# Kernel optimization log

Hardware: AMD Instinct MI355X
Metric: run time of the kernel (lower is better)

Reference implementation:

```python
import jax, jax.numpy as jnp
import numpy as np

H = 16        # num_attention_heads
DH = 64       # attention_head_dim
D = H * DH    # model dim = 1024
FF = 4 * D    # feed-forward inner dim = 4096
SCALE = DH ** -0.5
EPS = 1e-12


def _ln(x, g, b):
    m = jnp.mean(x, axis=-1, keepdims=True)
    v = jnp.mean((x - m) ** 2, axis=-1, keepdims=True)
    return (x - m) * jax.lax.rsqrt(v + EPS) * g + b


def _attn(x, ctx, Wq, Wk, Wv, Wo, bo, mask):
    # x: [B,S,D] (already pre-normed), ctx: [B,T,D], mask: [B,T] int (1=keep) or None
    B, S, _ = x.shape
    T = ctx.shape[1]
    q = (x @ Wq).reshape(B, S, H, DH)
    k = (ctx @ Wk).reshape(B, T, H, DH)
    v = (ctx @ Wv).reshape(B, T, H, DH)
    scores = jnp.einsum('bqhd,bkhd->bhqk', q, k) * SCALE  # [B,H,S,T]
    if mask is not None:
        scores = jnp.where(mask[:, None, None, :] == 0, -jnp.inf, scores)
    probs = jax.nn.softmax(scores, axis=-1)
    out = jnp.einsum('bhqk,bkhd->bqhd', probs, v).reshape(B, S, D)
    return out @ Wo + bo


def _geglu_ff(x, Wff1, bff1, Wff2, bff2):
    y = x @ Wff1 + bff1                 # [B,S,2*FF]
    h, gate = y[..., :FF], y[..., FF:]
    # GEGLU computes exact (erf) gelu in fp32
    g = jax.nn.gelu(gate.astype(jnp.float32), approximate=False).astype(gate.dtype)
    return (h * g) @ Wff2 + bff2


def setup_inputs() -> dict:
    key = jax.random.key(0)
    ks = jax.random.split(key, 24)
    B, S, T = 4, 1024, 1024
    w = lambda k, shp: jax.random.normal(k, shp, dtype=jnp.float32) * 0.02
    inp = {
        'hidden_states': jax.random.normal(ks[0], (B, S, D), dtype=jnp.float32),
        'context': jax.random.normal(ks[1], (B, T, D), dtype=jnp.float32),
        'encoder_key_padding_mask': jnp.ones((B, T), dtype=jnp.int32),
        'g1': jnp.ones((D,), jnp.float32), 'b1': jnp.zeros((D,), jnp.float32),
        'g2': jnp.ones((D,), jnp.float32), 'b2': jnp.zeros((D,), jnp.float32),
        'g3': jnp.ones((D,), jnp.float32), 'b3': jnp.zeros((D,), jnp.float32),
        'Wq1': w(ks[2], (D, D)), 'Wk1': w(ks[3], (D, D)), 'Wv1': w(ks[4], (D, D)),
        'Wo1': w(ks[5], (D, D)), 'bo1': jnp.zeros((D,), jnp.float32),
        'Wq2': w(ks[6], (D, D)), 'Wk2': w(ks[7], (D, D)), 'Wv2': w(ks[8], (D, D)),
        'Wo2': w(ks[9], (D, D)), 'bo2': jnp.zeros((D,), jnp.float32),
        'Wff1': w(ks[10], (D, 2 * FF)), 'bff1': jnp.zeros((2 * FF,), jnp.float32),
        'Wff2': w(ks[11], (FF, D)), 'bff2': jnp.zeros((D,), jnp.float32),
    }
    return inp


def reference(hidden_states, context, encoder_key_padding_mask,
              g1, b1, g2, b2, g3, b3,
              Wq1, Wk1, Wv1, Wo1, bo1,
              Wq2, Wk2, Wv2, Wo2, bo2,
              Wff1, bff1, Wff2, bff2):
    # Self-attention (attn1): context defaults to (normed) hidden_states, no padding mask
    n1 = _ln(hidden_states, g1, b1)
    h = hidden_states + _attn(n1, n1, Wq1, Wk1, Wv1, Wo1, bo1, None)
    # Cross-attention (attn2) with encoder key padding mask
    n2 = _ln(h, g2, b2)
    h = h + _attn(n2, context, Wq2, Wk2, Wv2, Wo2, bo2, encoder_key_padding_mask)
    # GEGLU feed-forward
    h = h + _geglu_ff(_ln(h, g3, b3), Wff1, bff1, Wff2, bff2)
    return h
```

## Files before the change

### kernel.cpp

```cpp
#include <hip/hip_runtime.h>

typedef unsigned short u16;
typedef unsigned int u32;

#define B_ 4
#define S_ 1024
#define D_ 1024
#define H_ 16
#define DH_ 64
#define FF_ 4096
#define M_ 4096
#define SCALE_ 0.125f

typedef __attribute__((ext_vector_type(8))) __bf16 bf16x8;
typedef __attribute__((ext_vector_type(4))) float f32x4;

__device__ __forceinline__ f32x4 mfma16(bf16x8 a, bf16x8 b, f32x4 c) {
  return __builtin_amdgcn_mfma_f32_16x16x32_bf16(a, b, c, 0, 0, 0);
}

__device__ __forceinline__ u16 f2bf(float x) {
  union { __bf16 h; u16 u; } cv; cv.h = (__bf16)x; return cv.u;
}
__device__ __forceinline__ float bf2f(u16 u) {
  union { u32 u; float f; } cv; cv.u = ((u32)u) << 16; return cv.f;
}
__device__ __forceinline__ u32 packbf2(float a, float b) {
  union { u32 u; __bf16 h[2]; } pk;
  pk.h[0] = (__bf16)a; pk.h[1] = (__bf16)b;
  return pk.u;
}
__device__ __forceinline__ float gelu_exact(float x) {
  return 0.5f * x * (1.f + erff(x * 0.7071067811865475f));
}
__device__ __forceinline__ void gload16(const void* g, void* l) {
  __builtin_amdgcn_global_load_lds((__attribute__((address_space(1))) void*)(g),
                                   (__attribute__((address_space(3))) void*)(l),
                                   16, 0, 0);
}

template<int EPI>
__global__ __launch_bounds__(256, 2) void gemm128(
    const u16* __restrict__ A, const u16* __restrict__ BT,
    const float* __restrict__ bias, const float* __restrict__ res,
    void* __restrict__ out, int M, int N, int K, int ktiles)
{
  __shared__ u16 As[2][128 * 64];
  __shared__ u16 Bs[2][128 * 64];

  const int tid = threadIdx.x;
  const int wave = tid >> 6, lane = tid & 63;
  const int wm = wave >> 1, wn = wave & 1;
  const int qi = lane & 15, g = lane >> 4;

  const int gx = N >> 7;
  const int nwg = gx * (M >> 7);
  int id = blockIdx.y * gridDim.x + blockIdx.x;
  id = (id & 7) * (nwg >> 3) + (id >> 3);
  const int m0 = (id / gx) << 7, n0 = (id % gx) << 7;

  const int NT = ktiles;
  const int kbase = blockIdx.z * ktiles * 64;

  const int r0 = tid >> 3;
  const int scol = (((tid & 7) ^ ((tid >> 3) & 7)) << 3);
  const int swb = wave << 6;

  f32x4 acc[4][4];
#pragma unroll
  for (int i = 0; i < 4; ++i)
#pragma unroll
    for (int j = 0; j < 4; ++j)
      acc[i][j] = (f32x4){0.f, 0.f, 0.f, 0.f};

#define STAGE_A(t, h, b) {                                                  \
    const int tt = (t) >= NT ? (t) - NT : (t);                              \
    _Pragma("unroll")                                                       \
    for (int i = 0; i < 2; ++i) {                                           \
      const int r = (h) * 64 + i * 32 + r0;                                 \
      gload16(A + (size_t)(m0 + r) * K + kbase + tt * 64 + scol,            \
              &As[b][(h) * 4096 + (i * 256 + swb) * 8]);                    \
    } }
#define STAGE_B(t, h, b) {                                                  \
    const int tt = (t) >= NT ? (t) - NT : (t);                              \
    _Pragma("unroll")                                                       \
    for (int i = 0; i < 2; ++i) {                                           \
      const int r = (h) * 64 + i * 32 + r0;                                 \
      gload16(BT + (size_t)(n0 + r) * K + kbase + tt * 64 + scol,           \
              &Bs[b][(h) * 4096 + (i * 256 + swb) * 8]);                    \
    } }

  bf16x8 af[4][2], bfr[4][2];

#define RD_ALL(b)                                                            \
  _Pragma("unroll") for (int mi = 0; mi < 4; ++mi)                           \
  _Pragma("unroll") for (int kk = 0; kk < 2; ++kk) {                         \
    const int row = wm * 64 + mi * 16 + qi;                                  \
    const int cb = ((kk * 64 + (g << 4)) ^ ((qi & 7) << 4));                 \
    af[mi][kk] = *(const bf16x8*)((const char*)&As[b][0] + row * 128 + cb);  \
  }                                                                          \
  _Pragma("unroll") for (int ni = 0; ni < 4; ++ni)                           \
  _Pragma("unroll") for (int kk = 0; kk < 2; ++kk) {                         \
    const int row = wn * 64 + ni * 16 + qi;                                  \
    const int cb = ((kk * 64 + (g << 4)) ^ ((qi & 7) << 4));                 \
    bfr[ni][kk] = *(const bf16x8*)((const char*)&Bs[b][0] + row * 128 + cb); \
  }

#define HALF(milo)                                                           \
  _Pragma("unroll") for (int mi = (milo); mi < (milo) + 2; ++mi)             \
  _Pragma("unroll") for (int ni = 0; ni < 4; ++ni)                           \
  _Pragma("unroll") for (int kk = 0; kk < 2; ++kk)                           \
    acc[mi][ni] = mfma16(af[mi][kk], bfr[ni][kk], acc[mi][ni]);

#define BAR() __builtin_amdgcn_s_barrier()
#define LGKM0() { asm volatile("s_waitcnt lgkmcnt(0)" ::: "memory");         \
                  __builtin_amdgcn_sched_barrier(0); }
#define VM8() asm volatile("s_waitcnt vmcnt(8)" ::: "memory")
#define PRIO(x) __builtin_amdgcn_s_setprio(x)

  STAGE_A(0, 0, 0); STAGE_A(0, 1, 0); STAGE_B(0, 0, 0); STAGE_B(0, 1, 0);
  STAGE_A(1, 0, 1); STAGE_A(1, 1, 1); STAGE_B(1, 0, 1); STAGE_B(1, 1, 1);
  VM8();
  BAR();

  const int NI = NT >> 1;
  for (int it = 0; it < NI; ++it) {
    const int k = it * 2;
    RD_ALL(0); LGKM0();
    BAR();
    STAGE_A(k + 2, 0, 0); STAGE_A(k + 2, 1, 0);
    PRIO(1); HALF(0); PRIO(0);
    STAGE_B(k + 2, 0, 0); STAGE_B(k + 2, 1, 0);
    PRIO(1); HALF(2); PRIO(0);
    VM8();
    BAR();
    RD_ALL(1); LGKM0();
    BAR();
    STAGE_A(k + 3, 0, 1); STAGE_A(k + 3, 1, 1);
    PRIO(1); HALF(0); PRIO(0);
    STAGE_B(k + 3, 0, 1); STAGE_B(k + 3, 1, 1);
    PRIO(1); HALF(2); PRIO(0);
    VM8();
    BAR();
  }

#pragma unroll
  for (int mi = 0; mi < 4; ++mi) {
#pragma unroll
    for (int ni = 0; ni < 4; ++ni) {
#pragma unroll
      for (int r = 0; r < 4; ++r) {
        const int m = m0 + wm * 64 + mi * 16 + g * 4 + r;
        const int n = n0 + wn * 64 + ni * 16 + qi;
        float v = acc[mi][ni][r];
        if (EPI == 0 || EPI == 5) {
          const int ts = n >> 10, b = m >> 10, s = m & 1023;
          const int hh = (n >> 6) & 15, dh = n & 63;
          if (EPI == 0 && ts == 0) v *= SCALE_;
          ((u16*)out)[(size_t)ts * (B_ * H_ * S_ * DH_) +
                      (((size_t)(b * H_ + hh) * S_) + s) * DH_ + dh] = f2bf(v);
        } else {
          const size_t idx = (size_t)m * N + n;
          ((float*)out)[idx] = res[idx] + v + bias[n];
        }
      }
    }
  }
#undef STAGE_A
#undef STAGE_B
#undef RD_ALL
#undef HALF
#undef BAR
#undef LGKM0
#undef VM8
#undef PRIO
}

__global__ __launch_bounds__(256, 2) void ffgeglu(
    const u16* __restrict__ A, const u16* __restrict__ BTh,
    const u16* __restrict__ BTg, const float* __restrict__ bias,
    u16* __restrict__ out)
{
  __shared__ u16 As[128 * 64];
  __shared__ u16 Bhs[128 * 64];
  __shared__ u16 Bgs[128 * 64];

  const int tid = threadIdx.x;
  const int wave = tid >> 6, lane = tid & 63;
  const int wm = wave >> 1, wn = wave & 1;
  const int qi = lane & 15, g = lane >> 4;

  const int gx = 32;
  const int nwg = 1024;
  int id = blockIdx.y * gridDim.x + blockIdx.x;
  id = (id & 7) * (nwg >> 3) + (id >> 3);
  const int m0 = (id / gx) << 7, n0 = (id % gx) << 7;
  const int K = 1024;

  const int r0 = tid >> 3;
  const int scol = (((tid & 7) ^ ((tid >> 3) & 7)) << 3);
  const int swb = wave << 6;

  f32x4 acch[4][4], accg[4][4];
#pragma unroll
  for (int i = 0; i < 4; ++i)
#pragma unroll
    for (int j = 0; j < 4; ++j) {
      acch[i][j] = (f32x4){0.f, 0.f, 0.f, 0.f};
      accg[i][j] = (f32x4){0.f, 0.f, 0.f, 0.f};
    }

  for (int t = 0; t < 16; ++t) {
    if (t) __syncthreads();
#pragma unroll
    for (int i = 0; i < 4; ++i) {
      const int r = i * 32 + r0;
      gload16(A + (size_t)(m0 + r) * K + t * 64 + scol,
              &As[(i * 256 + swb) * 8]);
    }
#pragma unroll
    for (int i = 0; i < 4; ++i) {
      const int r = i * 32 + r0;
      gload16(BTh + (size_t)(n0 + r) * K + t * 64 + scol,
              &Bhs[(i * 256 + swb) * 8]);
    }
#pragma unroll
    for (int i = 0; i < 4; ++i) {
      const int r = i * 32 + r0;
      gload16(BTg + (size_t)(n0 + r) * K + t * 64 + scol,
              &Bgs[(i * 256 + swb) * 8]);
    }
    __syncthreads();

    bf16x8 af[4][2], bfr[4][2];
#pragma unroll
    for (int mi = 0; mi < 4; ++mi)
#pragma unroll
      for (int kk = 0; kk < 2; ++kk) {
        const int row = wm * 64 + mi * 16 + qi;
        const int cb = ((kk * 64 + (g << 4)) ^ ((qi & 7) << 4));
        af[mi][kk] = *(const bf16x8*)((const char*)&As[0] + row * 128 + cb);
      }
#pragma unroll
    for (int ni = 0; ni < 4; ++ni)
#pragma unroll
      for (int kk = 0; kk < 2; ++kk) {
        const int row = wn * 64 + ni * 16 + qi;
        const int cb = ((kk * 64 + (g << 4)) ^ ((qi & 7) << 4));
        bfr[ni][kk] = *(const bf16x8*)((const char*)&Bhs[0] + row * 128 + cb);
      }
#pragma unroll
    for (int mi = 0; mi < 4; ++mi)
#pragma unroll
      for (int ni = 0; ni < 4; ++ni)
#pragma unroll
        for (int kk = 0; kk < 2; ++kk)
          acch[mi][ni] = mfma16(af[mi][kk], bfr[ni][kk], acch[mi][ni]);
#pragma unroll
    for (int ni = 0; ni < 4; ++ni)
#pragma unroll
      for (int kk = 0; kk < 2; ++kk) {
        const int row = wn * 64 + ni * 16 + qi;
        const int cb = ((kk * 64 + (g << 4)) ^ ((qi & 7) << 4));
        bfr[ni][kk] = *(const bf16x8*)((const char*)&Bgs[0] + row * 128 + cb);
      }
#pragma unroll
    for (int mi = 0; mi < 4; ++mi)
#pragma unroll
      for (int ni = 0; ni < 4; ++ni)
#pragma unroll
        for (int kk = 0; kk < 2; ++kk)
          accg[mi][ni] = mfma16(af[mi][kk], bfr[ni][kk], accg[mi][ni]);
  }

#pragma unroll
  for (int mi = 0; mi < 4; ++mi) {
#pragma unroll
    for (int ni = 0; ni < 4; ++ni) {
#pragma unroll
      for (int r = 0; r < 4; ++r) {
        const int m = m0 + wm * 64 + mi * 16 + g * 4 + r;
        const int n = n0 + wn * 64 + ni * 16 + qi;
        const float hv = acch[mi][ni][r] + bias[n];
        const float gv = accg[mi][ni][r] + bias[FF_ + n];
        out[(size_t)m * FF_ + n] = f2bf(hv * gelu_exact(gv));
      }
    }
  }
}

template<bool MASKED>
__global__ __launch_bounds__(256, 4) void attn_kernel(
    const u16* __restrict__ Q, const u16* __restrict__ Kb,
    const u16* __restrict__ VT, const float* __restrict__ bias,
    u16* __restrict__ O, int S, int T)
{
  __shared__ u16 Ks[64 * 72];
  __shared__ u16 VTs[64 * 72];
  __shared__ u16 Ps[4][16 * 72];
  __shared__ float biasS[64];

  const int bh = blockIdx.y;
  const int b = bh >> 4, h = bh & 15;
  const int tid = threadIdx.x;
  const int wave = tid >> 6, lane = tid & 63;
  const int g = lane >> 4, qi = lane & 15;
  const int q0w = blockIdx.x * 64 + wave * 16;

  const u16* Qb = Q + (size_t)bh * S * DH_;
  const u16* Kg = Kb + (size_t)bh * T * DH_;
  const u16* Vg = VT + (size_t)bh * DH_ * T;

  bf16x8 qf[2];
  qf[0] = *(const bf16x8*)&Qb[(q0w + qi) * DH_ + g * 8];
  qf[1] = *(const bf16x8*)&Qb[(q0w + qi) * DH_ + 32 + g * 8];

  f32x4 acc[4];
#pragma unroll
  for (int i = 0; i < 4; ++i) acc[i] = (f32x4){0.f, 0.f, 0.f, 0.f};
  float l_run = 1e-30f;

  u16* Pw = &Ps[wave][0];

  for (int t0 = 0; t0 < T; t0 += 64) {
    __syncthreads();
#pragma unroll
    for (int i = 0; i < 2; ++i) {
      const int flat = i * 256 + tid;
      const int row = flat >> 3, kc = flat & 7;
      *(uint4*)&Ks[row * 72 + kc * 8] = *(const uint4*)&Kg[(size_t)(t0 + row) * DH_ + kc * 8];
      *(uint4*)&VTs[row * 72 + kc * 8] = *(const uint4*)&Vg[(size_t)row * T + t0 + kc * 8];
    }
    if (MASKED && tid < 64) biasS[tid] = bias[b * T + t0 + tid];
    __syncthreads();

    f32x4 sacc[4];
#pragma unroll
    for (int nt = 0; nt < 4; ++nt) sacc[nt] = (f32x4){0.f, 0.f, 0.f, 0.f};
#pragma unroll
    for (int kk = 0; kk < 2; ++kk) {
#pragma unroll
      for (int nt = 0; nt < 4; ++nt) {
        bf16x8 kf = *(const bf16x8*)&Ks[(nt * 16 + qi) * 72 + kk * 32 + g * 8];
        sacc[nt] = mfma16(kf, qf[kk], sacc[nt]);
      }
    }
    float p[4][4];
    float lsum = 0.f;
#pragma unroll
    for (int nt = 0; nt < 4; ++nt)
#pragma unroll
      for (int r = 0; r < 4; ++r) {
        float v = sacc[nt][r];
        if (MASKED) v += biasS[nt * 16 + g * 4 + r];
        const float e = __expf(v);
        p[nt][r] = e;
        lsum += e;
      }
    lsum += __shfl_xor(lsum, 16);
    lsum += __shfl_xor(lsum, 32);
    l_run += lsum;

#pragma unroll
    for (int nt = 0; nt < 4; ++nt) {
      uint2 w;
      w.x = packbf2(p[nt][0], p[nt][1]);
      w.y = packbf2(p[nt][2], p[nt][3]);
      *(uint2*)&Pw[qi * 72 + nt * 16 + g * 4] = w;
    }

#pragma unroll
    for (int kk = 0; kk < 2; ++kk) {
      bf16x8 pf = *(const bf16x8*)&Pw[qi * 72 + kk * 32 + g * 8];
#pragma unroll
      for (int ndh = 0; ndh < 4; ++ndh) {
        bf16x8 vf = *(const bf16x8*)&VTs[(ndh * 16 + qi) * 72 + kk * 32 + g * 8];
        acc[ndh] = mfma16(vf, pf, acc[ndh]);
      }
    }
  }

  const float inv = 1.f / l_run;
  const int qg = q0w + qi;
#pragma unroll
  for (int ndh = 0; ndh < 4; ++ndh) {
    uint2 w;
    w.x = packbf2(acc[ndh][0] * inv, acc[ndh][1] * inv);
    w.y = packbf2(acc[ndh][2] * inv, acc[ndh][3] * inv);
    *(uint2*)&O[(size_t)(b * S_ + qg) * D_ + h * DH_ + ndh * 16 + g * 4] = w;
  }
}

__global__ __launch_bounds__(256) void ln_kernel(
    const float* __restrict__ x, const float* __restrict__ gg,
    const float* __restrict__ bb, u16* __restrict__ out)
{
  __shared__ float red[8];
  const int row = blockIdx.x, tid = threadIdx.x;
  const float4 v = ((const float4*)(x + (size_t)row * D_))[tid];
  float s = v.x + v.y + v.z + v.w;
  float sq = v.x * v.x + v.y * v.y + v.z * v.z + v.w * v.w;
#pragma unroll
  for (int m = 32; m; m >>= 1) {
    s += __shfl_xor(s, m);
    sq += __shfl_xor(sq, m);
  }
  const int wave = tid >> 6, lane = tid & 63;
  if (lane == 0) { red[wave * 2] = s; red[wave * 2 + 1] = sq; }
  __syncthreads();
  const float St = red[0] + red[2] + red[4] + red[6];
  const float SQt = red[1] + red[3] + red[5] + red[7];
  const float mean = St * (1.f / 1024.f);
  float var = SQt * (1.f / 1024.f) - mean * mean;
  var = fmaxf(var, 0.f);
  const float rinv = rsqrtf(var + 1e-12f);
  const float4 g4 = ((const float4*)gg)[tid];
  const float4 b4 = ((const float4*)bb)[tid];
  uint2 o;
  o.x = packbf2((v.x - mean) * rinv * g4.x + b4.x, (v.y - mean) * rinv * g4.y + b4.y);
  o.y = packbf2((v.z - mean) * rinv * g4.z + b4.z, (v.w - mean) * rinv * g4.w + b4.w);
  ((uint2*)(out + (size_t)row * D_))[tid] = o;
}

__global__ __launch_bounds__(256) void transpose_w(
    const float* __restrict__ in, u16* __restrict__ out, int K, int N)
{
  __shared__ float tile[32][33];
  const int tx = threadIdx.x & 31, ty = threadIdx.x >> 5;
  const int k0 = blockIdx.y * 32, n0 = blockIdx.x * 32;
#pragma unroll
  for (int j = 0; j < 4; ++j)
    tile[ty + 8 * j][tx] = in[(size_t)(k0 + ty + 8 * j) * N + n0 + tx];
  __syncthreads();
#pragma unroll
  for (int j = 0; j < 4; ++j)
    out[(size_t)(n0 + ty + 8 * j) * K + k0 + tx] = f2bf(tile[tx][ty + 8 * j]);
}

__global__ __launch_bounds__(256) void transpose_w8(
    const float* __restrict__ w0, const float* __restrict__ w1,
    const float* __restrict__ w2, const float* __restrict__ w3,
    const float* __restrict__ w4, const float* __restrict__ w5,
    const float* __restrict__ w6, const float* __restrict__ w7,
    u16* __restrict__ outbase)
{
  __shared__ float tile[32][33];
  const float* srcs[8] = {w0, w1, w2, w3, w4, w5, w6, w7};
  const float* in = srcs[blockIdx.z];
  u16* out = outbase + (size_t)blockIdx.z * 1024 * 1024;
  const int tx = threadIdx.x & 31, ty = threadIdx.x >> 5;
  const int k0 = blockIdx.y * 32, n0 = blockIdx.x * 32;
#pragma unroll
  for (int j = 0; j < 4; ++j)
    tile[ty + 8 * j][tx] = in[(size_t)(k0 + ty + 8 * j) * 1024 + n0 + tx];
  __syncthreads();
#pragma unroll
  for (int j = 0; j < 4; ++j)
    out[(size_t)(n0 + ty + 8 * j) * 1024 + k0 + tx] = f2bf(tile[tx][ty + 8 * j]);
}

__global__ __launch_bounds__(256) void transpose_v(
    const u16* __restrict__ in, u16* __restrict__ out, int T)
{
  __shared__ u16 tile[32][33];
  const int tx = threadIdx.x & 31, ty = threadIdx.x >> 5;
  const int bh = blockIdx.z;
  const int t0 = blockIdx.x * 32, d0 = blockIdx.y * 32;
  const u16* ib = in + (size_t)bh * T * DH_;
  u16* ob = out + (size_t)bh * DH_ * T;
#pragma unroll
  for (int j = 0; j < 4; ++j)
    tile[ty + 8 * j][tx] = ib[(size_t)(t0 + ty + 8 * j) * DH_ + d0 + tx];
  __syncthreads();
#pragma unroll
  for (int j = 0; j < 4; ++j)
    ob[(size_t)(d0 + ty + 8 * j) * T + t0 + tx] = tile[tx][ty + 8 * j];
}

__global__ void cvt_bf16(const float* __restrict__ in, u16* __restrict__ out, int n4)
{
  const int i = blockIdx.x * blockDim.x + threadIdx.x;
  if (i < n4) {
    const float4 v = ((const float4*)in)[i];
    uint2 o;
    o.x = packbf2(v.x, v.y);
    o.y = packbf2(v.z, v.w);
    ((uint2*)out)[i] = o;
  }
}

__global__ void mask_bias(const int* __restrict__ mask, float* __restrict__ bias, int n)
{
  const int i = blockIdx.x * blockDim.x + threadIdx.x;
  if (i < n) bias[i] = mask[i] ? 0.f : -1e30f;
}

extern "C" void kernel_launch(void* const* d_in, const int* in_sizes, int n_in,
                              void* d_out, int out_size, void* d_ws, size_t ws_size,
                              hipStream_t stream)
{
  (void)in_sizes; (void)n_in; (void)out_size; (void)ws_size;
  const float* hidden = (const float*)d_in[0];
  const float* ctx    = (const float*)d_in[1];
  const int*   mask   = (const int*)d_in[2];
  const float* g1 = (const float*)d_in[3];
  const float* b1 = (const float*)d_in[4];
  const float* g2 = (const float*)d_in[5];
  const float* b2 = (const float*)d_in[6];
  const float* g3 = (const float*)d_in[7];
  const float* b3 = (const float*)d_in[8];
  const float* Wq1 = (const float*)d_in[9];
  const float* Wk1 = (const float*)d_in[10];
  const float* Wv1 = (const float*)d_in[11];
  const float* Wo1 = (const float*)d_in[12];
  const float* bo1 = (const float*)d_in[13];
  const float* Wq2 = (const float*)d_in[14];
  const float* Wk2 = (const float*)d_in[15];
  const float* Wv2 = (const float*)d_in[16];
  const float* Wo2 = (const float*)d_in[17];
  const float* bo2 = (const float*)d_in[18];
  const float* Wff1 = (const float*)d_in[19];
  const float* bff1 = (const float*)d_in[20];
  const float* Wff2 = (const float*)d_in[21];
  const float* bff2 = (const float*)d_in[22];

  char* ws = (char*)d_ws;
  size_t off = 0;
  auto alloc = [&](size_t bytes) -> void* {
    void* p = ws + off;
    off += (bytes + 255) & ~(size_t)255;
    return p;
  };
  u16* WqT1  = (u16*)alloc((size_t)1024 * 1024 * 2);
  u16* WkT1  = (u16*)alloc((size_t)1024 * 1024 * 2);
  u16* WvT1  = (u16*)alloc((size_t)1024 * 1024 * 2);
  u16* WoT1  = (u16*)alloc((size_t)1024 * 1024 * 2);
  u16* WqT2  = (u16*)alloc((size_t)1024 * 1024 * 2);
  u16* WkT2  = (u16*)alloc((size_t)1024 * 1024 * 2);
  u16* WvT2  = (u16*)alloc((size_t)1024 * 1024 * 2);
  u16* WoT2  = (u16*)alloc((size_t)1024 * 1024 * 2);
  u16* Wff1T = (u16*)alloc((size_t)8192 * 1024 * 2);
  u16* Wff2T = (u16*)alloc((size_t)1024 * 4096 * 2);
  u16* nbuf  = (u16*)alloc((size_t)M_ * D_ * 2);
  u16* hgbuf = (u16*)alloc((size_t)M_ * FF_ * 2);
  u16* qbuf  = (u16*)alloc((size_t)M_ * D_ * 2);
  u16* kbuf  = (u16*)alloc((size_t)M_ * D_ * 2);
  u16* vbuf  = (u16*)alloc((size_t)M_ * D_ * 2);
  u16* vtbuf = (u16*)alloc((size_t)M_ * D_ * 2);
  u16* attnb = (u16*)alloc((size_t)M_ * D_ * 2);
  u16* ctxb  = (u16*)alloc((size_t)M_ * D_ * 2);
  float* biasw = (float*)alloc((size_t)B_ * S_ * 4);
  float* hres = (float*)d_out;
  (void)WkT1; (void)WvT1; (void)WkT2; (void)WvT2; (void)WoT2;

  const dim3 blk(256);
  const dim3 gW8(32, 32, 8);
  const dim3 gQKV(24, 32);
  const dim3 gKV(16, 32);
  const dim3 gP(8, 32);
  const dim3 gFF(32, 32);
  const dim3 gA(16, 64);
  const dim3 gV(32, 2, 64);

  transpose_w8<<<gW8, blk, 0, stream>>>(Wq1, Wk1, Wv1, Wo1, Wq2, Wk2, Wv2, Wo2,
                                        WqT1);
  transpose_w<<<dim3(256, 32), blk, 0, stream>>>(Wff1, Wff1T, 1024, 8192);
  transpose_w<<<dim3(32, 128), blk, 0, stream>>>(Wff2, Wff2T, 4096, 1024);
  cvt_bf16<<<dim3(4096), blk, 0, stream>>>(ctx, ctxb, 1048576);
  mask_bias<<<dim3(16), blk, 0, stream>>>(mask, biasw, B_ * S_);

  ln_kernel<<<dim3(M_), blk, 0, stream>>>(hidden, g1, b1, nbuf);
  gemm128<0><<<gQKV, blk, 0, stream>>>(nbuf, WqT1, nullptr, nullptr,
                                       qbuf, M_, 3072, 1024, 16);
  transpose_v<<<gV, blk, 0, stream>>>(vbuf, vtbuf, 1024);
  attn_kernel<false><<<gA, blk, 0, stream>>>(qbuf, kbuf, vtbuf, nullptr, attnb,
                                             S_, S_);
  gemm128<1><<<gP, blk, 0, stream>>>(attnb, WoT1, bo1, hidden,
                                     hres, M_, 1024, 1024, 16);
  ln_kernel<<<dim3(M_), blk, 0, stream>>>(hres, g2, b2, nbuf);

  gemm128<0><<<gP, blk, 0, stream>>>(nbuf, WqT2, nullptr, nullptr,
                                     qbuf, M_, 1024, 1024, 16);
  gemm128<5><<<gKV, blk, 0, stream>>>(ctxb, WkT2, nullptr, nullptr,
                                      kbuf, M_, 2048, 1024, 16);
  transpose_v<<<gV, blk, 0, stream>>>(vbuf, vtbuf, 1024);
  attn_kernel<true><<<gA, blk, 0, stream>>>(qbuf, kbuf, vtbuf, biasw, attnb,
                                            S_, S_);
  gemm128<1><<<gP, blk, 0, stream>>>(attnb, WoT2, bo2, hres,
                                     hres, M_, 1024, 1024, 16);
  ln_kernel<<<dim3(M_), blk, 0, stream>>>(hres, g3, b3, nbuf);

  ffgeglu<<<gFF, blk, 0, stream>>>(nbuf, Wff1T, Wff1T + (size_t)FF_ * 1024,
                                   bff1, hgbuf);
  gemm128<1><<<gP, blk, 0, stream>>>(hgbuf, Wff2T, bff2, hres,
                                     hres, M_, 1024, 4096, 64);
}
```

Before: 361.4 us.

## Split-K the output projections and fuse bias, residual and LayerNorm into a reduction

The Wo1, Wo2 and Wff2 GEMMs, which have N=1024 and only 256 tiles, now run split-K across blockIdx.z (2 or 4 slices) and write bf16 partial sums. A new reduce_ln kernel sums the partials, adds bias and residual, and optionally applies the following LayerNorm in the same pass, replacing the separate ln_kernel launches. This raises GPU occupancy for the small-grid GEMMs at the cost of extra partial-buffer traffic and bf16 rounding of partial sums. The ffgeglu launch bound is also raised to 3 blocks per SM.

```diff
diff --git a/kernel.cpp b/kernel.cpp
--- a/kernel.cpp
+++ b/kernel.cpp
@@ -159,9 +159,13 @@
           if (EPI == 0 && ts == 0) v *= SCALE_;
           ((u16*)out)[(size_t)ts * (B_ * H_ * S_ * DH_) +
                       (((size_t)(b * H_ + hh) * S_) + s) * DH_ + dh] = f2bf(v);
-        } else {
+        } else if (EPI == 1) {
           const size_t idx = (size_t)m * N + n;
           ((float*)out)[idx] = res[idx] + v + bias[n];
+        } else {
+          const size_t idx = (size_t)blockIdx.z * ((size_t)M * N) +
+                             (size_t)m * N + n;
+          ((u16*)out)[idx] = f2bf(v);
         }
       }
     }
@@ -176,7 +180,7 @@
 #undef PRIO
 }
 
-__global__ __launch_bounds__(256, 2) void ffgeglu(
+__global__ __launch_bounds__(256, 3) void ffgeglu(
     const u16* __restrict__ A, const u16* __restrict__ BTh,
     const u16* __restrict__ BTg, const float* __restrict__ bias,
     u16* __restrict__ out)
@@ -286,6 +290,63 @@
         out[(size_t)m * FF_ + n] = f2bf(hv * gelu_exact(gv));
       }
     }
+  }
+}
+
+template<bool DOLN, int NS>
+__global__ __launch_bounds__(256) void reduce_ln(
+    const u16* __restrict__ p, const float* __restrict__ bias,
+    const float* __restrict__ res, float* __restrict__ outf,
+    const float* __restrict__ gg, const float* __restrict__ bb,
+    u16* __restrict__ outn)
+{
+  __shared__ float red[8];
+  const int row = blockIdx.x, tid = threadIdx.x;
+  const size_t base = (size_t)row * 1024 + tid * 4;
+  const size_t total = (size_t)M_ * 1024;
+  float a0 = 0.f, a1 = 0.f, a2 = 0.f, a3 = 0.f;
+#pragma unroll
+  for (int s = 0; s < NS; ++s) {
+    const uint2 u = *(const uint2*)&p[(size_t)s * total + base];
+    a0 += bf2f((u16)(u.x & 0xffff));
+    a1 += bf2f((u16)(u.x >> 16));
+    a2 += bf2f((u16)(u.y & 0xffff));
+    a3 += bf2f((u16)(u.y >> 16));
+  }
+  const float4 b4 = ((const float4*)bias)[tid];
+  const float4 r4 = *(const float4*)&res[base];
+  float4 o;
+  o.x = r4.x + a0 + b4.x;
+  o.y = r4.y + a1 + b4.y;
+  o.z = r4.z + a2 + b4.z;
+  o.w = r4.w + a3 + b4.w;
+  *(float4*)&outf[base] = o;
+
+  if (DOLN) {
+    float s1 = o.x + o.y + o.z + o.w;
+    float s2 = o.x * o.x + o.y * o.y + o.z * o.z + o.w * o.w;
+#pragma unroll
+    for (int m = 32; m; m >>= 1) {
+      s1 += __shfl_xor(s1, m);
+      s2 += __shfl_xor(s2, m);
+    }
+    const int wave = tid >> 6, lane = tid & 63;
+    if (lane == 0) { red[wave * 2] = s1; red[wave * 2 + 1] = s2; }
+    __syncthreads();
+    const float St = red[0] + red[2] + red[4] + red[6];
+    const float SQt = red[1] + red[3] + red[5] + red[7];
+    const float mean = St * (1.f / 1024.f);
+    float var = SQt * (1.f / 1024.f) - mean * mean;
+    var = fmaxf(var, 0.f);
+    const float rinv = rsqrtf(var + 1e-12f);
+    const float4 g4 = ((const float4*)gg)[tid];
+    const float4 bb4 = ((const float4*)bb)[tid];
+    uint2 w;
+    w.x = packbf2((o.x - mean) * rinv * g4.x + bb4.x,
+                  (o.y - mean) * rinv * g4.y + bb4.y);
+    w.y = packbf2((o.z - mean) * rinv * g4.z + bb4.z,
+                  (o.w - mean) * rinv * g4.w + bb4.w);
+    ((uint2*)(outn + (size_t)row * 1024))[tid] = w;
   }
 }
 
@@ -549,6 +610,7 @@
   u16* vtbuf = (u16*)alloc((size_t)M_ * D_ * 2);
   u16* attnb = (u16*)alloc((size_t)M_ * D_ * 2);
   u16* ctxb  = (u16*)alloc((size_t)M_ * D_ * 2);
+  u16* pbuf  = (u16*)alloc((size_t)4 * M_ * D_ * 2);
   float* biasw = (float*)alloc((size_t)B_ * S_ * 4);
   float* hres = (float*)d_out;
   (void)WkT1; (void)WvT1; (void)WkT2; (void)WvT2; (void)WoT2;
@@ -558,9 +620,12 @@
   const dim3 gQKV(24, 32);
   const dim3 gKV(16, 32);
   const dim3 gP(8, 32);
+  const dim3 gS2(8, 32, 2);
+  const dim3 gF4(8, 32, 4);
   const dim3 gFF(32, 32);
   const dim3 gA(16, 64);
   const dim3 gV(32, 2, 64);
+  const dim3 gR(4096);
 
   transpose_w8<<<gW8, blk, 0, stream>>>(Wq1, Wk1, Wv1, Wo1, Wq2, Wk2, Wv2, Wo2,
                                         WqT1);
@@ -575,9 +640,9 @@
   transpose_v<<<gV, blk, 0, stream>>>(vbuf, vtbuf, 1024);
   attn_kernel<false><<<gA, blk, 0, stream>>>(qbuf, kbuf, vtbuf, nullptr, attnb,
                                              S_, S_);
-  gemm128<1><<<gP, blk, 0, stream>>>(attnb, WoT1, bo1, hidden,
-                                     hres, M_, 1024, 1024, 16);
-  ln_kernel<<<dim3(M_), blk, 0, stream>>>(hres, g2, b2, nbuf);
+  gemm128<4><<<gS2, blk, 0, stream>>>(attnb, WoT1, nullptr, nullptr,
+                                      pbuf, M_, 1024, 1024, 8);
+  reduce_ln<true, 2><<<gR, blk, 0, stream>>>(pbuf, bo1, hidden, hres, g2, b2, nbuf);
 
   gemm128<0><<<gP, blk, 0, stream>>>(nbuf, WqT2, nullptr, nullptr,
                                      qbuf, M_, 1024, 1024, 16);
@@ -586,12 +651,14 @@
   transpose_v<<<gV, blk, 0, stream>>>(vbuf, vtbuf, 1024);
   attn_kernel<true><<<gA, blk, 0, stream>>>(qbuf, kbuf, vtbuf, biasw, attnb,
                                             S_, S_);
-  gemm128<1><<<gP, blk, 0, stream>>>(attnb, WoT2, bo2, hres,
-                                     hres, M_, 1024, 1024, 16);
-  ln_kernel<<<dim3(M_), blk, 0, stream>>>(hres, g3, b3, nbuf);
+  gemm128<4><<<gS2, blk, 0, stream>>>(attnb, WoT2, nullptr, nullptr,
+                                      pbuf, M_, 1024, 1024, 8);
+  reduce_ln<true, 2><<<gR, blk, 0, stream>>>(pbuf, bo2, hres, hres, g3, b3, nbuf);
 
   ffgeglu<<<gFF, blk, 0, stream>>>(nbuf, Wff1T, Wff1T + (size_t)FF_ * 1024,
                                    bff1, hgbuf);
-  gemm128<1><<<gP, blk, 0, stream>>>(hgbuf, Wff2T, bff2, hres,
-                                     hres, M_, 1024, 4096, 64);
-}
+  gemm128<4><<<gF4, blk, 0, stream>>>(hgbuf, Wff2T, nullptr, nullptr,
+                                      pbuf, M_, 1024, 4096, 16);
+  reduce_ln<false, 4><<<gR, blk, 0, stream>>>(pbuf, bff2, hres, hres, nullptr,
+                                              nullptr, nullptr);
+}
```

Measured after the change: 587.3 us. 1.62x slower.
